# Kernel tuning notes

Measured on AMD Instinct MI355X. Metric: run time of the kernel, lower is better.

Reference implementation:

```python
import jax, jax.numpy as jnp
import numpy as np

N, E, B = 4096, 4096, 128  # nodes, edges, graphs


def _param(key, shape, scale):
    return jax.random.normal(key, shape, dtype=jnp.float32) * scale


def setup_inputs() -> dict:
    key = jax.random.key(0)
    ks = jax.random.split(key, 32)
    inp = {
        "x": jax.random.normal(ks[0], (N, 37), dtype=jnp.float32),
        "edge_index": jax.random.randint(ks[1], (2, E), 0, N),
        "edge_attr": jax.random.uniform(ks[2], (E, 5), dtype=jnp.float32),
        "batch": jnp.sort(jax.random.randint(ks[3], (N,), 0, B)),
        # NNConv 1: edge-MLP 5->512->37*128, root [37,128]
        "nn1_w1": _param(ks[4], (5, 512), 0.3),
        "nn1_b1": jnp.zeros((512,), jnp.float32),
        "nn1_w2": _param(ks[5], (512, 37 * 128), 0.01),
        "nn1_b2": jnp.zeros((37 * 128,), jnp.float32),
        "root1": _param(ks[6], (37, 128), 0.1),
        "bias1": jnp.zeros((128,), jnp.float32),
        # NNConv 2: edge-MLP 5->128->128*256, root [128,256]
        "nn2_w1": _param(ks[7], (5, 128), 0.3),
        "nn2_b1": jnp.zeros((128,), jnp.float32),
        "nn2_w2": _param(ks[8], (128, 128 * 256), 0.005),
        "nn2_b2": jnp.zeros((128 * 256,), jnp.float32),
        "root2": _param(ks[9], (128, 256), 0.05),
        "bias2": jnp.zeros((256,), jnp.float32),
        # NNConv 3: edge-MLP 5->128->256*256, root [256,256]
        "nn3_w1": _param(ks[10], (5, 128), 0.3),
        "nn3_b1": jnp.zeros((128,), jnp.float32),
        "nn3_w2": _param(ks[11], (128, 256 * 256), 0.005),
        "nn3_b2": jnp.zeros((256 * 256,), jnp.float32),
        "root3": _param(ks[12], (256, 256), 0.05),
        "bias3": jnp.zeros((256,), jnp.float32),
        # readout MLP
        "fc1_w": _param(ks[13], (256, 128), 0.06),
        "fc1_b": jnp.zeros((128,), jnp.float32),
        "fc2_w": _param(ks[14], (128, 64), 0.09),
        "fc2_b": jnp.zeros((64,), jnp.float32),
        "fc3_w": _param(ks[15], (64, 1), 0.12),
        "fc3_b": jnp.zeros((1,), jnp.float32),
    }
    return inp


def _nnconv(x, src, dst, edge_attr, w1, b1, w2, b2, root, bias, cin, cout):
    # edge MLP -> per-edge weight matrix [E, cin, cout]
    h = jax.nn.relu(edge_attr @ w1 + b1)
    W = (h @ w2 + b2).reshape(-1, cin, cout)
    # gather source features, per-edge matvec, scatter-add to targets
    msg = jnp.einsum('ei,eio->eo', x[src], W)          # [E, cout]
    agg = jax.ops.segment_sum(msg, dst, num_segments=x.shape[0])
    return agg + x @ root + bias


def _segment_mean(x, seg, num_segments):
    s = jax.ops.segment_sum(x, seg, num_segments=num_segments)
    cnt = jax.ops.segment_sum(jnp.ones((x.shape[0],), x.dtype), seg,
                              num_segments=num_segments)
    return s / jnp.maximum(cnt, 1.0)[:, None]


def reference(x, edge_index, edge_attr, batch,
              nn1_w1, nn1_b1, nn1_w2, nn1_b2, root1, bias1,
              nn2_w1, nn2_b1, nn2_w2, nn2_b2, root2, bias2,
              nn3_w1, nn3_b1, nn3_w2, nn3_b2, root3, bias3,
              fc1_w, fc1_b, fc2_w, fc2_b, fc3_w, fc3_b):
    src, dst = edge_index[0], edge_index[1]
    h = jax.nn.elu(_nnconv(x, src, dst, edge_attr, nn1_w1, nn1_b1, nn1_w2,
                           nn1_b2, root1, bias1, 37, 128))
    h = jax.nn.elu(_nnconv(h, src, dst, edge_attr, nn2_w1, nn2_b1, nn2_w2,
                           nn2_b2, root2, bias2, 128, 256))
    h = jax.nn.elu(_nnconv(h, src, dst, edge_attr, nn3_w1, nn3_b1, nn3_w2,
                           nn3_b2, root3, bias3, 256, 256))
    g = _segment_mean(h, batch, B)                     # [B, 256]
    g = jax.nn.elu(g @ fc1_w + fc1_b)
    g = jax.nn.elu(g @ fc2_w + fc2_b)
    g = g @ fc3_w + fc3_b
    return g.reshape(-1)
```

## Files before the change

### kernel.cpp

```cpp
#include <hip/hip_runtime.h>
#include <cstdint>
#include <cstddef>

typedef float f32x4 __attribute__((ext_vector_type(4)));
typedef _Float16 f16x8 __attribute__((ext_vector_type(8)));
typedef _Float16 f16x4 __attribute__((ext_vector_type(4)));

__device__ __forceinline__ float elu_f(float x) { return x > 0.f ? x : expm1f(x); }

__device__ __forceinline__ void gload_lds16(const void* g, void* l)
{
    __builtin_amdgcn_global_load_lds(
        (const __attribute__((address_space(1))) void*)g,
        (__attribute__((address_space(3))) void*)l,
        16, 0, 0);
}

template <int CIN, int COUT, int KFTOT>
__device__ __forceinline__
void pack_body(int bid, int tid, const float* __restrict__ w2, const float* __restrict__ b2,
               _Float16* __restrict__ w2h, int KH, float* tile )
{
    const int kh = bid / KFTOT;
    const int c  = bid - kh * KFTOT;
    const int CP = 32 * COUT;
    for (int i = tid; i < CP; i += 256) {
        int kk = i / COUT, n = i - kk * COUT;
        int kg = c * 32 + kk;
        float v = 0.f;
        if (kg < CIN) v = (kh < KH) ? w2[((size_t)kh * CIN + kg) * COUT + n]
                                    : b2[(size_t)kg * COUT + n];
        tile[kk * (COUT + 2) + n] = v;
    }
    __syncthreads();
    _Float16* outp = w2h + (size_t)bid * CP;
    for (int i = tid; i < CP; i += 256) {
        int n = i >> 5, kk = i & 31;
        int blk = (kk >> 3) ^ ((n >> 1) & 3);
        outp[n * 32 + blk * 8 + (kk & 7)] = (_Float16)tile[kk * (COUT + 2) + n];
    }
}

__global__ __launch_bounds__(256)
void uber_prologue_kernel(const float* __restrict__ ea,
                          const int* __restrict__ dst, int* __restrict__ cnt,
                          const float* __restrict__ w1a, const float* __restrict__ b1a, _Float16* __restrict__ h1T,
                          const float* __restrict__ w1b, const float* __restrict__ b1b, _Float16* __restrict__ h2T,
                          const float* __restrict__ w1c, const float* __restrict__ b1c, _Float16* __restrict__ h3T,
                          int E,
                          const float* __restrict__ w2a, const float* __restrict__ b2a, _Float16* __restrict__ w2h1,
                          const float* __restrict__ w2b, const float* __restrict__ b2b, _Float16* __restrict__ w2h2,
                          const float* __restrict__ w2c, const float* __restrict__ b2c, _Float16* __restrict__ w2h3)
{
    __shared__ __align__(16) float smem[32 * 258];
    const int tid = threadIdx.x;
    const int nEB = E >> 6;
    int b = blockIdx.x;

    if (b < nEB) {
        const int e0 = b * 64;
        const int el = tid & 63;
        const int cg = tid >> 6;
        if (tid < 64) atomicAdd(&cnt[dst[e0 + tid]], 1);
        float* a = smem;
        for (int i = tid; i < 320; i += 256) a[(i / 5) * 5 + (i % 5)] = ea[e0 * 5 + i];
        __syncthreads();
        float av[5];
        #pragma unroll
        for (int j = 0; j < 5; ++j) av[j] = a[el * 5 + j];
        #pragma unroll 4
        for (int t = 0; t < 128; ++t) {
            const int ch = t * 4 + cg;
            float s = b1a[ch];
            #pragma unroll
            for (int j = 0; j < 5; ++j) s = fmaf(av[j], w1a[j * 512 + ch], s);
            h1T[(size_t)ch * E + e0 + el] = (_Float16)fmaxf(s, 0.f);
        }
        #pragma unroll 4
        for (int t = 0; t < 32; ++t) {
            const int ch = t * 4 + cg;
            float s = b1b[ch];
            float u = b1c[ch];
            #pragma unroll
            for (int j = 0; j < 5; ++j) {
                s = fmaf(av[j], w1b[j * 128 + ch], s);
                u = fmaf(av[j], w1c[j * 128 + ch], u);
            }
            h2T[(size_t)ch * E + e0 + el] = (_Float16)fmaxf(s, 0.f);
            h3T[(size_t)ch * E + e0 + el] = (_Float16)fmaxf(u, 0.f);
        }
        return;
    }
    b -= nEB;
    if (b < 513 * 2) { pack_body<37, 128, 2>(b, tid, w2a, b2a, w2h1, 512, smem); return; }
    b -= 513 * 2;
    if (b < 129 * 4) { pack_body<128, 256, 4>(b, tid, w2b, b2b, w2h2, 128, smem); return; }
    b -= 129 * 4;
    pack_body<256, 256, 8>(b, tid, w2c, b2c, w2h3, 128, smem);
}

__global__ __launch_bounds__(256)
void csr_scan_graph_kernel(const int* __restrict__ cnt, int* __restrict__ offs, int N,
                           const int* __restrict__ batch, int* __restrict__ goffs, int B,
                           int NN)
{
    __shared__ int sums[256];
    __shared__ int pref[257];
    const int tid = threadIdx.x;
    const int per = N / 256;
    int loc = 0;
    for (int i = 0; i < per; ++i) loc += cnt[tid * per + i];
    sums[tid] = loc;
    __syncthreads();
    if (tid == 0) {
        int s = 0; pref[0] = 0;
        for (int i = 0; i < 256; ++i) { s += sums[i]; pref[i + 1] = s; }
    }
    __syncthreads();
    int run = pref[tid];
    for (int i = 0; i < per; ++i) { offs[tid * per + i] = run; run += cnt[tid * per + i]; }
    if (tid == 255) offs[N] = run;
    for (int g = tid; g <= B; g += 256) {
        int lo = 0, hi = NN;
        while (lo < hi) { int mid = (lo + hi) >> 1; if (batch[mid] < g) lo = mid + 1; else hi = mid; }
        goffs[g] = lo;
    }
}

__global__ __launch_bounds__(256)
void csr_fill_kernel(const int* __restrict__ dst, const int* __restrict__ offs,
                     int* __restrict__ cur, int* __restrict__ eid, int E)
{
    int e = blockIdx.x * 256 + threadIdx.x;
    if (e < E) {
        int d = dst[e];
        int p = offs[d] + atomicAdd(&cur[d], 1);
        eid[p] = e;
    }
}

template <int KH, int CIN, int COUT, int KFTOT, int CSPLIT, int NY>
__global__ __launch_bounds__(256, 2)
void msg_mfma_kernel(const float* __restrict__ xin,
                     const _Float16* __restrict__ hT,
                     const _Float16* __restrict__ w2h,
                     const int* __restrict__ src,
                     _Float16* __restrict__ part,
                     int E, int khg_per)
{
    constexpr int BM = 512;
    constexpr int KF = KFTOT / CSPLIT;
    static_assert(KF == 1, "mf=8 msg kernel expects one 32-k chunk per block");

    __shared__ __align__(16) _Float16 bsh[2][64][32];
    __shared__ int s_src[BM];

    const int tid  = threadIdx.x;
    const int lane = tid & 63;
    const int w    = tid >> 6;
    const int l15  = lane & 15;
    const int lg   = lane >> 4;
    const int swb  = (l15 >> 1) & 3;

    const int nwg = gridDim.x;
    const int bid = blockIdx.x;
    const int swz = (bid & 7) * (nwg >> 3) + (bid >> 3);
    const int m    = swz & 7;
    const int rest = swz >> 3;
    const int y    = rest % NY;
    const int zz   = rest / NY;
    const int cinH = zz % CSPLIT;
    const int zkh  = zz / CSPLIT;

    const int e0  = m * BM;
    const int n0  = y * 64;
    const int k0  = cinH * 32;
    const int kh0 = zkh * khg_per;
    const int kh1 = min(kh0 + khg_per, KH + 1);

    s_src[tid]       = src[e0 + tid];
    s_src[tid + 256] = src[e0 + tid + 256];
    __syncthreads();

    f16x8 a_[8];
    #pragma unroll
    for (int mf = 0; mf < 8; ++mf) {
        const int eloc = w * 128 + mf * 16 + l15;
        const float* xrow = xin + (size_t)s_src[eloc] * CIN + k0;
        if (CIN % 32 == 0) {
            float4 p0 = *(const float4*)(xrow + lg * 8);
            float4 p1 = *(const float4*)(xrow + lg * 8 + 4);
            a_[mf][0] = (_Float16)p0.x; a_[mf][1] = (_Float16)p0.y;
            a_[mf][2] = (_Float16)p0.z; a_[mf][3] = (_Float16)p0.w;
            a_[mf][4] = (_Float16)p1.x; a_[mf][5] = (_Float16)p1.y;
            a_[mf][6] = (_Float16)p1.z; a_[mf][7] = (_Float16)p1.w;
        } else {
            #pragma unroll
            for (int j = 0; j < 8; ++j) {
                int kk = lg * 8 + j;
                float v = (k0 + kk < CIN) ? xrow[kk] : 0.f;
                a_[mf][j] = (_Float16)v;
            }
        }
    }

    f32x4 msg[8][4];
    #pragma unroll
    for (int mf = 0; mf < 8; ++mf)
        #pragma unroll
        for (int nf = 0; nf < 4; ++nf) msg[mf][nf] = 0.f;

    auto stage = [&](int khg, int pp) {
        if (khg >= kh1) return;
        const size_t chunk = (size_t)khg * KFTOT + cinH;
        const char* g = (const char*)(w2h + (chunk * COUT + n0) * 32) + (size_t)tid * 16;
        char* l = (char*)(&bsh[pp][0][0]) + (tid >> 6) * 1024;
        gload_lds16(g, l);
    };

    stage(kh0, 0);

    int p = 0;
    for (int khg = kh0; khg < kh1; ++khg) {
        __syncthreads();

        stage(khg + 1, p ^ 1);

        _Float16 hh[8];
        if (khg < KH) {
            const _Float16* hp = hT + (size_t)khg * E + e0 + w * 128 + l15;
            #pragma unroll
            for (int mf = 0; mf < 8; ++mf) hh[mf] = hp[mf * 16];
        } else {
            #pragma unroll
            for (int mf = 0; mf < 8; ++mf) hh[mf] = (_Float16)1.0f;
        }

        f16x8 Bv[4];
        #pragma unroll
        for (int nf = 0; nf < 4; ++nf)
            Bv[nf] = *(const f16x8*)&bsh[p][nf * 16 + l15][(lg ^ swb) * 8];

        #pragma unroll
        for (int mf = 0; mf < 8; ++mf) {
            f16x8 ah = a_[mf] * hh[mf];
            #pragma unroll
            for (int nf = 0; nf < 4; ++nf)
                msg[mf][nf] = __builtin_amdgcn_mfma_f32_16x16x32_f16(ah, Bv[nf], msg[mf][nf], 0, 0, 0);
        }
        p ^= 1;
    }

    _Float16* pb = part + ((size_t)zz * E + e0) * COUT + n0;
    #pragma unroll
    for (int mf = 0; mf < 8; ++mf)
        #pragma unroll
        for (int r = 0; r < 4; ++r) {
            const int row = w * 128 + mf * 16 + lg * 4 + r;
            #pragma unroll
            for (int nf = 0; nf < 4; ++nf)
                pb[(size_t)row * COUT + nf * 16 + l15] = (_Float16)msg[mf][nf][r];
        }
}

template <int CIN, int COUT, int Z>
__global__ __launch_bounds__(256)
void node_gemm_kernel(const float* __restrict__ xin,
                      const float* __restrict__ root,
                      const _Float16* __restrict__ part,
                      const int* __restrict__ offs,
                      const int* __restrict__ eid,
                      const float* __restrict__ bias,
                      float* __restrict__ out, int E)
{
    constexpr int BM  = 64;
    constexpr int BN  = 64;
    constexpr int BKI = (CIN % 32 == 0) ? 32 : 16;
    constexpr int CIN_PAD = ((CIN + BKI - 1) / BKI) * BKI;
    constexpr int CPK = CIN_PAD / BKI;
    constexpr int NROWS = BKI / 16;

    __shared__ __align__(16) float xs_t[CIN_PAD][BM];
    __shared__ __align__(16) float btile[BKI][BN];

    const int tid = threadIdx.x;
    const int tx  = tid & 15;
    const int ty  = tid >> 4;
    const int ty4 = ty * 4;
    const int tx4 = tx * 4;
    const int e0  = blockIdx.x * BM;
    const int n0  = blockIdx.y * BN;

    for (int idx = tid; idx < BM * CIN_PAD; idx += 256) {
        int mm = idx / CIN_PAD;
        int i  = idx - mm * CIN_PAD;
        float v = 0.f;
        if (i < CIN) v = xin[(size_t)(e0 + mm) * CIN + i];
        xs_t[i][mm] = v;
    }

    const int rbase = tid >> 4;
    const int nn    = (tid & 15) * 4;
    float acc[4][4] = {};
    float4 pre[NROWS];

    {
        const float* brow = root + n0;
        #pragma unroll
        for (int rr = 0; rr < NROWS; ++rr) {
            int r = rbase + rr * 16;
            float4 v = {0.f, 0.f, 0.f, 0.f};
            if (r < CIN) v = *(const float4*)(brow + (size_t)r * COUT + nn);
            pre[rr] = v;
        }
    }

    for (int c = 0; c < CPK; ++c) {
        __syncthreads();
        #pragma unroll
        for (int rr = 0; rr < NROWS; ++rr)
            *(float4*)&btile[rbase + rr * 16][nn] = pre[rr];
        __syncthreads();

        if (c + 1 < CPK) {
            int i0n = (c + 1) * BKI;
            const float* brow = root + (size_t)i0n * COUT + n0;
            #pragma unroll
            for (int rr = 0; rr < NROWS; ++rr) {
                int r = rbase + rr * 16;
                float4 v = {0.f, 0.f, 0.f, 0.f};
                if (i0n + r < CIN) v = *(const float4*)(brow + (size_t)r * COUT + nn);
                pre[rr] = v;
            }
        }

        const int i0 = c * BKI;
        #pragma unroll
        for (int ii = 0; ii < BKI; ++ii) {
            float4 xv = *(const float4*)&xs_t[i0 + ii][ty4];
            float4 bv = *(const float4*)&btile[ii][tx4];
            float av[4] = {xv.x, xv.y, xv.z, xv.w};
            float bvv[4] = {bv.x, bv.y, bv.z, bv.w};
            #pragma unroll
            for (int mm = 0; mm < 4; ++mm)
                #pragma unroll
                for (int nq = 0; nq < 4; ++nq)
                    acc[mm][nq] = fmaf(av[mm], bvv[nq], acc[mm][nq]);
        }
    }

    float bs[4];
    #pragma unroll
    for (int nq = 0; nq < 4; ++nq) bs[nq] = bias[n0 + tx4 + nq];

    #pragma unroll
    for (int mm = 0; mm < 4; ++mm) {
        const int row = e0 + ty4 + mm;
        float add[4] = {0.f, 0.f, 0.f, 0.f};
        const int b = offs[row], t = offs[row + 1];
        for (int j = b; j < t; ++j) {
            const int e = eid[j];
            #pragma unroll
            for (int z = 0; z < Z; ++z) {
                f16x4 r4 = *(const f16x4*)(part + ((size_t)z * E + e) * COUT + n0 + tx4);
                add[0] += (float)r4.x; add[1] += (float)r4.y;
                add[2] += (float)r4.z; add[3] += (float)r4.w;
            }
        }
        size_t base = (size_t)row * COUT + n0 + tx4;
        #pragma unroll
        for (int nq = 0; nq < 4; ++nq)
            out[base + nq] = elu_f(acc[mm][nq] + add[nq] + bs[nq]);
    }
}

__global__ __launch_bounds__(256)
void pool_readout_kernel(const float* __restrict__ hl3, const int* __restrict__ goffs,
                         const float* __restrict__ fc1w, const float* __restrict__ fc1b,
                         const float* __restrict__ fc2w, const float* __restrict__ fc2b,
                         const float* __restrict__ fc3w, const float* __restrict__ fc3b,
                         float* __restrict__ outp)
{
    const int g   = blockIdx.x;
    const int tid = threadIdx.x;
    __shared__ float gm[256];
    __shared__ float a1[128];
    __shared__ float a2[64];
    const int b = goffs[g], t = goffs[g + 1];
    float s = 0.f;
    for (int n = b; n < t; ++n) s += hl3[(size_t)n * 256 + tid];
    gm[tid] = s / fmaxf((float)(t - b), 1.f);
    __syncthreads();
    if (tid < 128) {
        float v = fc1b[tid];
        for (int j = 0; j < 256; ++j) v = fmaf(gm[j], fc1w[j * 128 + tid], v);
        a1[tid] = elu_f(v);
    }
    __syncthreads();
    if (tid < 64) {
        float v = fc2b[tid];
        for (int j = 0; j < 128; ++j) v = fmaf(a1[j], fc2w[j * 64 + tid], v);
        a2[tid] = elu_f(v);
    }
    __syncthreads();
    if (tid == 0) {
        float v = fc3b[0];
        for (int j = 0; j < 64; ++j) v = fmaf(a2[j], fc3w[j], v);
        outp[g] = v;
    }
}

extern "C" void kernel_launch(void* const* d_in, const int* in_sizes, int n_in,
                              void* d_out, int out_size, void* d_ws, size_t ws_size,
                              hipStream_t stream)
{
    const float* x      = (const float*)d_in[0];
    const int*   ei     = (const int*)  d_in[1];
    const float* ea     = (const float*)d_in[2];
    const int*   batch  = (const int*)  d_in[3];
    const float* nn1_w1 = (const float*)d_in[4];
    const float* nn1_b1 = (const float*)d_in[5];
    const float* nn1_w2 = (const float*)d_in[6];
    const float* nn1_b2 = (const float*)d_in[7];
    const float* root1  = (const float*)d_in[8];
    const float* bias1  = (const float*)d_in[9];
    const float* nn2_w1 = (const float*)d_in[10];
    const float* nn2_b1 = (const float*)d_in[11];
    const float* nn2_w2 = (const float*)d_in[12];
    const float* nn2_b2 = (const float*)d_in[13];
    const float* root2  = (const float*)d_in[14];
    const float* bias2  = (const float*)d_in[15];
    const float* nn3_w1 = (const float*)d_in[16];
    const float* nn3_b1 = (const float*)d_in[17];
    const float* nn3_w2 = (const float*)d_in[18];
    const float* nn3_b2 = (const float*)d_in[19];
    const float* root3  = (const float*)d_in[20];
    const float* bias3  = (const float*)d_in[21];
    const float* fc1_w  = (const float*)d_in[22];
    const float* fc1_b  = (const float*)d_in[23];
    const float* fc2_w  = (const float*)d_in[24];
    const float* fc2_b  = (const float*)d_in[25];
    const float* fc3_w  = (const float*)d_in[26];
    const float* fc3_b  = (const float*)d_in[27];

    const int E = in_sizes[2] / 5;
    const int N = in_sizes[0] / 37;
    const int B = out_size;
    const int* srcp = ei;
    const int* dstp = ei + E;

    const size_t W1H = (size_t)513 * 2 * 128 * 32;
    const size_t W2H = (size_t)129 * 4 * 256 * 32;
    const size_t W3H = (size_t)129 * 8 * 256 * 32;
    _Float16* w2h1 = (_Float16*)d_ws;
    _Float16* w2h2 = w2h1 + W1H;
    _Float16* w2h3 = w2h2 + W2H;
    _Float16* h1T  = w2h3 + W3H;
    _Float16* h2T  = h1T + (size_t)512 * E;
    _Float16* h3T  = h2T + (size_t)128 * E;
    _Float16* part = h3T + (size_t)128 * E;
    float* fbase = (float*)(part + (size_t)32 * E * 128);
    float* hl1   = fbase;
    float* hl2   = hl1 + (size_t)N * 128;
    float* hl3   = hl2 + (size_t)N * 256;
    int* ibase   = (int*)(hl3 + (size_t)N * 256);
    int* cnt   = ibase;
    int* cur   = cnt + N;
    int* offs  = cur + N;
    int* eid   = offs + N + 1;
    int* goffs = eid + E;

    hipMemsetAsync(cnt, 0, 2 * N * sizeof(int), stream);

    const int nEB = E / 64;
    uber_prologue_kernel<<<nEB + 1026 + 516 + 1032, 256, 0, stream>>>(
        ea, dstp, cnt,
        nn1_w1, nn1_b1, h1T, nn2_w1, nn2_b1, h2T, nn3_w1, nn3_b1, h3T, E,
        nn1_w2, nn1_b2, w2h1, nn2_w2, nn2_b2, w2h2, nn3_w2, nn3_b2, w2h3);

    csr_scan_graph_kernel<<<1, 256, 0, stream>>>(cnt, offs, N, batch, goffs, B, N);
    csr_fill_kernel<<<(E + 255) / 256, 256, 0, stream>>>(dstp, offs, cur, eid, E);

    msg_mfma_kernel<512, 37, 128, 2, 2, 2><<<512, 256, 0, stream>>>(
        x, h1T, w2h1, srcp, part, E, 33);
    node_gemm_kernel<37, 128, 32><<<dim3(N / 64, 2), 256, 0, stream>>>(
        x, root1, part, offs, eid, bias1, hl1, E);

    msg_mfma_kernel<128, 128, 256, 4, 4, 4><<<512, 256, 0, stream>>>(
        hl1, h2T, w2h2, srcp, part, E, 33);
    node_gemm_kernel<128, 256, 16><<<dim3(N / 64, 4), 256, 0, stream>>>(
        hl1, root2, part, offs, eid, bias2, hl2, E);

    msg_mfma_kernel<128, 256, 256, 8, 8, 4><<<512, 256, 0, stream>>>(
        hl2, h3T, w2h3, srcp, part, E, 65);
    node_gemm_kernel<256, 256, 16><<<dim3(N / 64, 4), 256, 0, stream>>>(
        hl2, root3, part, offs, eid, bias3, hl3, E);

    pool_readout_kernel<<<B, 256, 0, stream>>>(hl3, goffs, fc1_w, fc1_b,
                                               fc2_w, fc2_b, fc3_w, fc3_b,
                                               (float*)d_out);
}
```

Before: 297.8 us.

## Give each wave a private weight tile copy and drop block barriers

Each wave now loads its own copy of the shared 64x32 weight tile into a per-wave LDS slice (four 16-byte loads per lane) instead of splitting one tile across the block. That removes the __syncthreads per k-step in favour of a per-wave vmcnt wait. The loop is also unrolled by two with register double-buffering of the h values, so the next step's loads are issued before the MFMAs. The cost is four times the LDS footprint and four times the global-to-LDS traffic for weights, which could hurt occupancy or bandwidth.

```diff
diff --git a/kernel.cpp b/kernel.cpp
--- a/kernel.cpp
+++ b/kernel.cpp
@@ -150,9 +150,9 @@
 {
     constexpr int BM = 512;
     constexpr int KF = KFTOT / CSPLIT;
-    static_assert(KF == 1, "mf=8 msg kernel expects one 32-k chunk per block");
-
-    __shared__ __align__(16) _Float16 bsh[2][64][32];
+    static_assert(KF == 1, "per-wave msg kernel expects one 32-k chunk per block");
+
+    __shared__ __align__(16) _Float16 bsh[2][4][64][32];
     __shared__ int s_src[BM];
 
     const int tid  = threadIdx.x;
@@ -211,22 +211,14 @@
         for (int nf = 0; nf < 4; ++nf) msg[mf][nf] = 0.f;
 
     auto stage = [&](int khg, int pp) {
-        if (khg >= kh1) return;
         const size_t chunk = (size_t)khg * KFTOT + cinH;
-        const char* g = (const char*)(w2h + (chunk * COUT + n0) * 32) + (size_t)tid * 16;
-        char* l = (char*)(&bsh[pp][0][0]) + (tid >> 6) * 1024;
-        gload_lds16(g, l);
+        const char* g = (const char*)(w2h + (chunk * COUT + n0) * 32) + (size_t)lane * 16;
+        char* l = (char*)(&bsh[pp][w][0][0]);
+        #pragma unroll
+        for (int i = 0; i < 4; ++i)
+            gload_lds16(g + i * 1024, l + i * 1024);
     };
-
-    stage(kh0, 0);
-
-    int p = 0;
-    for (int khg = kh0; khg < kh1; ++khg) {
-        __syncthreads();
-
-        stage(khg + 1, p ^ 1);
-
-        _Float16 hh[8];
+    auto load_h = [&](int khg, _Float16* hh) {
         if (khg < KH) {
             const _Float16* hp = hT + (size_t)khg * E + e0 + w * 128 + l15;
             #pragma unroll
@@ -235,21 +227,38 @@
             #pragma unroll
             for (int mf = 0; mf < 8; ++mf) hh[mf] = (_Float16)1.0f;
         }
-
+    };
+
+    _Float16 hA[8], hB[8];
+    load_h(kh0, hA);
+    stage(kh0, 0);
+
+    auto iter = [&](int khg, const _Float16* hc, _Float16* hn, int pp) {
+        asm volatile("s_waitcnt vmcnt(0)" ::: "memory");
+        __builtin_amdgcn_sched_barrier(0);
         f16x8 Bv[4];
         #pragma unroll
         for (int nf = 0; nf < 4; ++nf)
-            Bv[nf] = *(const f16x8*)&bsh[p][nf * 16 + l15][(lg ^ swb) * 8];
-
+            Bv[nf] = *(const f16x8*)&bsh[pp][w][nf * 16 + l15][(lg ^ swb) * 8];
+        if (khg + 1 < kh1) {
+            load_h(khg + 1, hn);
+            stage(khg + 1, pp ^ 1);
+        }
         #pragma unroll
         for (int mf = 0; mf < 8; ++mf) {
-            f16x8 ah = a_[mf] * hh[mf];
+            f16x8 ah = a_[mf] * hc[mf];
             #pragma unroll
             for (int nf = 0; nf < 4; ++nf)
                 msg[mf][nf] = __builtin_amdgcn_mfma_f32_16x16x32_f16(ah, Bv[nf], msg[mf][nf], 0, 0, 0);
         }
-        p ^= 1;
-    }
+    };
+
+    int khg = kh0;
+    for (; khg + 1 < kh1; khg += 2) {
+        iter(khg,     hA, hB, 0);
+        iter(khg + 1, hB, hA, 1);
+    }
+    if (khg < kh1) iter(khg, hA, hB, 0);
 
     _Float16* pb = part + ((size_t)zz * E + e0) * COUT + n0;
     #pragma unroll
```

After: 298.7 us. Within noise of the previous version (+0.3%).

## Replace FP32 scalar root GEMM in node kernel with split-bf16 MFMA

Applied to the files above, without the earlier changes.

The node kernel's root-weight GEMM moves from FP32 FMAs on the vector ALUs to bf16 16x16x32 MFMA instructions. To keep close to FP32 accuracy, each operand is split into a high and a low bf16 part and three MFMA products are summed. Tiles are staged in swizzled LDS, and the accumulators are written back through shared memory so the existing CSR gather and ELU epilogue can stay as they were. This cuts vector-ALU time for the dense part, at the cost of extra conversion work, three MFMAs per product, and a small loss of precision.

```diff
diff --git a/kernel.cpp b/kernel.cpp
--- a/kernel.cpp
+++ b/kernel.cpp
@@ -5,8 +5,17 @@
 typedef float f32x4 __attribute__((ext_vector_type(4)));
 typedef _Float16 f16x8 __attribute__((ext_vector_type(8)));
 typedef _Float16 f16x4 __attribute__((ext_vector_type(4)));
+typedef short s16x8 __attribute__((ext_vector_type(8)));
 
 __device__ __forceinline__ float elu_f(float x) { return x > 0.f ? x : expm1f(x); }
+
+__device__ __forceinline__ unsigned short f2bf(float f) {
+    unsigned u = __float_as_uint(f);
+    return (unsigned short)((u + 0x7FFFu + ((u >> 16) & 1u)) >> 16);
+}
+__device__ __forceinline__ float bf2f(unsigned short b) {
+    return __uint_as_float(((unsigned)b) << 16);
+}
 
 __device__ __forceinline__ void gload_lds16(const void* g, void* l)
 {
@@ -264,8 +273,8 @@
 }
 
 template <int CIN, int COUT, int Z>
-__global__ __launch_bounds__(256)
-void node_gemm_kernel(const float* __restrict__ xin,
+__global__ __launch_bounds__(256, 2)
+void node_mfma_kernel(const float* __restrict__ xin,
                       const float* __restrict__ root,
                       const _Float16* __restrict__ part,
                       const int* __restrict__ offs,
@@ -273,81 +282,124 @@
                       const float* __restrict__ bias,
                       float* __restrict__ out, int E)
 {
-    constexpr int BM  = 64;
-    constexpr int BN  = 64;
-    constexpr int BKI = (CIN % 32 == 0) ? 32 : 16;
-    constexpr int CIN_PAD = ((CIN + BKI - 1) / BKI) * BKI;
-    constexpr int CPK = CIN_PAD / BKI;
-    constexpr int NROWS = BKI / 16;
-
-    __shared__ __align__(16) float xs_t[CIN_PAD][BM];
-    __shared__ __align__(16) float btile[BKI][BN];
-
-    const int tid = threadIdx.x;
+    constexpr int KC    = (CIN + 31) / 32;
+    constexpr int NSTEP = KC / 2;
+
+    __shared__ __align__(16) char smem[32768];
+    short (*ash)[2][64][32] = (short (*)[2][64][32])smem;
+    short (*bsh)[2][64][32] = (short (*)[2][64][32])(smem + 16384);
+    float (*csh)[68]        = (float (*)[68])smem;
+
+    const int tid  = threadIdx.x;
+    const int lane = tid & 63;
+    const int w    = tid >> 6;
+    const int l15  = lane & 15;
+    const int lg   = lane >> 4;
+    const int swb  = (l15 >> 1) & 3;
+    const int e0   = blockIdx.x * 64;
+    const int n0   = blockIdx.y * 64;
+
+    f32x4 ahh[4], alh[4], ahl[4];
+    #pragma unroll
+    for (int nf = 0; nf < 4; ++nf) { ahh[nf] = 0.f; alh[nf] = 0.f; ahl[nf] = 0.f; }
+
+    const int srow = tid & 63;
+    const int sco  = (tid >> 6) * 16;
+
+    for (int s = 0; s < NSTEP; ++s) {
+        __syncthreads();
+
+        {
+            const int kbase = s * 64 + sco;
+            float v[16];
+            if (CIN % 64 == 0) {
+                const float* xr = xin + (size_t)(e0 + srow) * CIN + kbase;
+                float4 q0 = *(const float4*)(xr + 0);
+                float4 q1 = *(const float4*)(xr + 4);
+                float4 q2 = *(const float4*)(xr + 8);
+                float4 q3 = *(const float4*)(xr + 12);
+                v[0]=q0.x; v[1]=q0.y; v[2]=q0.z; v[3]=q0.w;
+                v[4]=q1.x; v[5]=q1.y; v[6]=q1.z; v[7]=q1.w;
+                v[8]=q2.x; v[9]=q2.y; v[10]=q2.z; v[11]=q2.w;
+                v[12]=q3.x; v[13]=q3.y; v[14]=q3.z; v[15]=q3.w;
+            } else {
+                const float* xr = xin + (size_t)(e0 + srow) * CIN;
+                #pragma unroll
+                for (int j = 0; j < 16; ++j)
+                    v[j] = (kbase + j < CIN) ? xr[kbase + j] : 0.f;
+            }
+            #pragma unroll
+            for (int g = 0; g < 2; ++g) {
+                const int ko = sco + g * 8;
+                const int cs = (ko >> 5) & 1;
+                const int kb = (ko >> 3) & 3;
+                const int blk = kb ^ ((srow >> 1) & 3);
+                s16x8 h8, l8;
+                #pragma unroll
+                for (int j = 0; j < 8; ++j) {
+                    unsigned short hb = f2bf(v[g * 8 + j]);
+                    h8[j] = (short)hb;
+                    l8[j] = (short)f2bf(v[g * 8 + j] - bf2f(hb));
+                }
+                *(s16x8*)&ash[cs][0][srow][blk * 8] = h8;
+                *(s16x8*)&ash[cs][1][srow][blk * 8] = l8;
+            }
+        }
+        {
+            float v[16];
+            #pragma unroll
+            for (int j = 0; j < 16; ++j) {
+                const int k = s * 64 + sco + j;
+                v[j] = (k < CIN) ? root[(size_t)k * COUT + n0 + srow] : 0.f;
+            }
+            #pragma unroll
+            for (int g = 0; g < 2; ++g) {
+                const int ko = sco + g * 8;
+                const int cs = (ko >> 5) & 1;
+                const int kb = (ko >> 3) & 3;
+                const int blk = kb ^ ((srow >> 1) & 3);
+                s16x8 h8, l8;
+                #pragma unroll
+                for (int j = 0; j < 8; ++j) {
+                    unsigned short hb = f2bf(v[g * 8 + j]);
+                    h8[j] = (short)hb;
+                    l8[j] = (short)f2bf(v[g * 8 + j] - bf2f(hb));
+                }
+                *(s16x8*)&bsh[cs][0][srow][blk * 8] = h8;
+                *(s16x8*)&bsh[cs][1][srow][blk * 8] = l8;
+            }
+        }
+        __syncthreads();
+
+        #pragma unroll
+        for (int cs = 0; cs < 2; ++cs) {
+            const int arow = w * 16 + l15;
+            s16x8 Ah = *(const s16x8*)&ash[cs][0][arow][(lg ^ swb) * 8];
+            s16x8 Al = *(const s16x8*)&ash[cs][1][arow][(lg ^ swb) * 8];
+            #pragma unroll
+            for (int nf = 0; nf < 4; ++nf) {
+                const int bcol = nf * 16 + l15;
+                s16x8 Bh = *(const s16x8*)&bsh[cs][0][bcol][(lg ^ swb) * 8];
+                s16x8 Bl = *(const s16x8*)&bsh[cs][1][bcol][(lg ^ swb) * 8];
+                ahh[nf] = __builtin_amdgcn_mfma_f32_16x16x32_bf16(Ah, Bh, ahh[nf], 0, 0, 0);
+                alh[nf] = __builtin_amdgcn_mfma_f32_16x16x32_bf16(Al, Bh, alh[nf], 0, 0, 0);
+                ahl[nf] = __builtin_amdgcn_mfma_f32_16x16x32_bf16(Ah, Bl, ahl[nf], 0, 0, 0);
+            }
+        }
+    }
+
+    __syncthreads();
+    #pragma unroll
+    for (int nf = 0; nf < 4; ++nf)
+        #pragma unroll
+        for (int r = 0; r < 4; ++r)
+            csh[w * 16 + lg * 4 + r][nf * 16 + l15] = ahh[nf][r] + alh[nf][r] + ahl[nf][r];
+    __syncthreads();
+
     const int tx  = tid & 15;
     const int ty  = tid >> 4;
     const int ty4 = ty * 4;
     const int tx4 = tx * 4;
-    const int e0  = blockIdx.x * BM;
-    const int n0  = blockIdx.y * BN;
-
-    for (int idx = tid; idx < BM * CIN_PAD; idx += 256) {
-        int mm = idx / CIN_PAD;
-        int i  = idx - mm * CIN_PAD;
-        float v = 0.f;
-        if (i < CIN) v = xin[(size_t)(e0 + mm) * CIN + i];
-        xs_t[i][mm] = v;
-    }
-
-    const int rbase = tid >> 4;
-    const int nn    = (tid & 15) * 4;
-    float acc[4][4] = {};
-    float4 pre[NROWS];
-
-    {
-        const float* brow = root + n0;
-        #pragma unroll
-        for (int rr = 0; rr < NROWS; ++rr) {
-            int r = rbase + rr * 16;
-            float4 v = {0.f, 0.f, 0.f, 0.f};
-            if (r < CIN) v = *(const float4*)(brow + (size_t)r * COUT + nn);
-            pre[rr] = v;
-        }
-    }
-
-    for (int c = 0; c < CPK; ++c) {
-        __syncthreads();
-        #pragma unroll
-        for (int rr = 0; rr < NROWS; ++rr)
-            *(float4*)&btile[rbase + rr * 16][nn] = pre[rr];
-        __syncthreads();
-
-        if (c + 1 < CPK) {
-            int i0n = (c + 1) * BKI;
-            const float* brow = root + (size_t)i0n * COUT + n0;
-            #pragma unroll
-            for (int rr = 0; rr < NROWS; ++rr) {
-                int r = rbase + rr * 16;
-                float4 v = {0.f, 0.f, 0.f, 0.f};
-                if (i0n + r < CIN) v = *(const float4*)(brow + (size_t)r * COUT + nn);
-                pre[rr] = v;
-            }
-        }
-
-        const int i0 = c * BKI;
-        #pragma unroll
-        for (int ii = 0; ii < BKI; ++ii) {
-            float4 xv = *(const float4*)&xs_t[i0 + ii][ty4];
-            float4 bv = *(const float4*)&btile[ii][tx4];
-            float av[4] = {xv.x, xv.y, xv.z, xv.w};
-            float bvv[4] = {bv.x, bv.y, bv.z, bv.w};
-            #pragma unroll
-            for (int mm = 0; mm < 4; ++mm)
-                #pragma unroll
-                for (int nq = 0; nq < 4; ++nq)
-                    acc[mm][nq] = fmaf(av[mm], bvv[nq], acc[mm][nq]);
-        }
-    }
 
     float bs[4];
     #pragma unroll
@@ -370,7 +422,7 @@
         size_t base = (size_t)row * COUT + n0 + tx4;
         #pragma unroll
         for (int nq = 0; nq < 4; ++nq)
-            out[base + nq] = elu_f(acc[mm][nq] + add[nq] + bs[nq]);
+            out[base + nq] = elu_f(csh[ty4 + mm][tx4 + nq] + add[nq] + bs[nq]);
     }
 }
 
@@ -483,17 +535,17 @@
 
     msg_mfma_kernel<512, 37, 128, 2, 2, 2><<<512, 256, 0, stream>>>(
         x, h1T, w2h1, srcp, part, E, 33);
-    node_gemm_kernel<37, 128, 32><<<dim3(N / 64, 2), 256, 0, stream>>>(
+    node_mfma_kernel<37, 128, 32><<<dim3(N / 64, 2), 256, 0, stream>>>(
         x, root1, part, offs, eid, bias1, hl1, E);
 
     msg_mfma_kernel<128, 128, 256, 4, 4, 4><<<512, 256, 0, stream>>>(
         hl1, h2T, w2h2, srcp, part, E, 33);
-    node_gemm_kernel<128, 256, 16><<<dim3(N / 64, 4), 256, 0, stream>>>(
+    node_mfma_kernel<128, 256, 16><<<dim3(N / 64, 4), 256, 0, stream>>>(
         hl1, root2, part, offs, eid, bias2, hl2, E);
 
     msg_mfma_kernel<128, 256, 256, 8, 8, 4><<<512, 256, 0, stream>>>(
         hl2, h3T, w2h3, srcp, part, E, 65);
-    node_gemm_kernel<256, 256, 16><<<dim3(N / 64, 4), 256, 0, stream>>>(
+    node_mfma_kernel<256, 256, 16><<<dim3(N / 64, 4), 256, 0, stream>>>(
         hl2, root3, part, offs, eid, bias3, hl3, E);
 
     pool_readout_kernel<<<B, 256, 0, stream>>>(hl3, goffs, fc1_w, fc1_b,
```

New measurement: 280.8 us (median of 2 runs). 1.06x faster.
